# Optimization experiments

Measured on AMD Instinct MI355X. Metric: run time of the kernel, lower is better.

Reference implementation:

```python
import jax, jax.numpy as jnp
import numpy as np

N = 100000      # nodes
E = 3200000     # edges (avg degree 32)
F_IN = 16       # node_feature_size
R1, R2, R3 = 8, 16, 8   # gcn hidden sizes
N1 = 32                  # mlp hidden


def _lin(k, fan_in, shape):
    s = 1.0 / np.sqrt(fan_in)
    return jax.random.uniform(k, shape, minval=-s, maxval=s, dtype=jnp.float32)


def setup_inputs() -> dict:
    key = jax.random.key(0)
    ks = jax.random.split(key, 16)
    x = jax.random.normal(ks[0], (N, F_IN), dtype=jnp.float32)
    edge_index = jax.random.randint(ks[1], (2, E), 0, N, dtype=jnp.int64)
    return {
        "x": x,
        "edge_index": edge_index,
        # GraphConv k: out = mean_agg(x_j) @ W_rel + b + x @ W_root  (PyG GraphConv, lin_root bias=False)
        "W_rel1": _lin(ks[2], F_IN, (F_IN, R1)), "b1": _lin(ks[3], F_IN, (R1,)), "W_root1": _lin(ks[4], F_IN, (F_IN, R1)),
        "W_rel2": _lin(ks[5], R1, (R1, R2)),   "b2": _lin(ks[6], R1, (R2,)),   "W_root2": _lin(ks[7], R1, (R1, R2)),
        "W_rel3": _lin(ks[8], R2, (R2, R3)),   "b3": _lin(ks[9], R2, (R3,)),   "W_root3": _lin(ks[10], R2, (R2, R3)),
        "fc1_W": _lin(ks[11], R3, (R3, N1)), "fc1_b": _lin(ks[12], R3, (N1,)),
        "fc2_W": _lin(ks[13], N1, (N1, 1)),  "fc2_b": _lin(ks[14], N1, (1,)),
    }


def _graph_conv(x, src, dst, W_rel, b, W_root):
    # message: gather source features; aggregate: mean over incoming edges at dst
    n = x.shape[0]
    msg_sum = jax.ops.segment_sum(x[src], dst, num_segments=n)          # [N, F]
    cnt = jax.ops.segment_sum(jnp.ones(src.shape, x.dtype), dst, num_segments=n)
    mean = msg_sum / jnp.maximum(cnt, 1.0)[:, None]
    return mean @ W_rel + b + x @ W_root


def reference(x, edge_index, W_rel1, b1, W_root1, W_rel2, b2, W_root2,
              W_rel3, b3, W_root3, fc1_W, fc1_b, fc2_W, fc2_b):
    src, dst = edge_index[0], edge_index[1]
    h = jax.nn.sigmoid(_graph_conv(x, src, dst, W_rel1, b1, W_root1))
    h = jax.nn.sigmoid(_graph_conv(h, src, dst, W_rel2, b2, W_root2))
    h = jax.nn.sigmoid(_graph_conv(h, src, dst, W_rel3, b3, W_root3))
    h = jax.nn.sigmoid(h @ fc1_W + fc1_b)
    return h @ fc2_W + fc2_b   # [N, 1]
```

## Files before the change

### kernel.cpp

```cpp
#include <hip/hip_runtime.h>
#include <math.h>


#define CHUNK  8192
#define BW     128
#define MAXB   6144
#define MAXNB  800
#define MAXBLK 512

typedef _Float16 half8 __attribute__((ext_vector_type(8)));

static __device__ __forceinline__ float sigmoidf_(float x) {
    return 1.0f / (1.0f + expf(-x));
}

static __device__ __forceinline__ int scan256_excl(int v, int* s) {
    int tid = threadIdx.x;
    s[tid] = v;
    for (int off = 1; off < 256; off <<= 1) {
        __syncthreads();
        int t = (tid >= off) ? s[tid - off] : 0;
        __syncthreads();
        s[tid] += t;
    }
    __syncthreads();
    return s[tid] - v;
}

static __device__ __forceinline__ void gather_mean8(
    const half8* __restrict__ t, const int* __restrict__ csr,
    int rs, int d, float* s) {
#pragma unroll
    for (int c = 0; c < 8; ++c) s[c] = 0.0f;
    int e = 0;
    for (; e + 4 <= d; e += 4) {
        int4 ci = *(const int4*)(csr + rs + e);
        half8 v0 = t[ci.x]; half8 v1 = t[ci.y];
        half8 v2 = t[ci.z]; half8 v3 = t[ci.w];
#pragma unroll
        for (int c = 0; c < 8; ++c)
            s[c] += ((float)v0[c] + (float)v1[c]) + ((float)v2[c] + (float)v3[c]);
    }
    for (; e < d; ++e) {
        half8 v = t[csr[rs + e]];
#pragma unroll
        for (int c = 0; c < 8; ++c) s[c] += (float)v[c];
    }
    float inv = 1.0f / (float)(d > 0 ? d : 1);
#pragma unroll
    for (int c = 0; c < 8; ++c) s[c] *= inv;
}

__global__ __launch_bounds__(256)
void transform1_kernel(const float* __restrict__ x, const float* __restrict__ Wrel,
                       const float* __restrict__ bias, const float* __restrict__ Wroot,
                       _Float16* __restrict__ t1, _Float16* __restrict__ z1, int n) {
    __shared__ float sWr[128], sWo[128], sb[8];
    int tid = threadIdx.x;
    if (tid < 128) { sWr[tid] = Wrel[tid]; sWo[tid] = Wroot[tid]; }
    if (tid < 8) sb[tid] = bias[tid];
    __syncthreads();
    int node = blockIdx.x * 256 + tid;
    if (node >= n) return;
    const float4* x4 = (const float4*)x;
    float xv[16];
#pragma unroll
    for (int k = 0; k < 4; ++k) {
        float4 v = x4[node * 4 + k];
        xv[4 * k] = v.x; xv[4 * k + 1] = v.y; xv[4 * k + 2] = v.z; xv[4 * k + 3] = v.w;
    }
    float ta[8], za[8];
#pragma unroll
    for (int j = 0; j < 8; ++j) { ta[j] = 0.0f; za[j] = sb[j]; }
#pragma unroll
    for (int f = 0; f < 16; ++f) {
        float xf = xv[f];
#pragma unroll
        for (int j = 0; j < 8; ++j) {
            ta[j] += xf * sWr[f * 8 + j];
            za[j] += xf * sWo[f * 8 + j];
        }
    }
    half8 th, zh;
#pragma unroll
    for (int j = 0; j < 8; ++j) { th[j] = (_Float16)ta[j]; zh[j] = (_Float16)za[j]; }
    ((half8*)t1)[node] = th;
    ((half8*)z1)[node] = zh;
}

__global__ __launch_bounds__(256)
void bin_sort_kernel(const int* __restrict__ src, const int* __restrict__ dst,
                     unsigned* __restrict__ packed, int* __restrict__ counts_bm,
                     int* __restrict__ lstart_bm, int E, int NB) {
    __shared__ int s_hist[MAXNB];
    __shared__ int s_cur[MAXNB];
    __shared__ unsigned s_pk[CHUNK];
    __shared__ int s_scan[256];
    int tid = threadIdx.x, blk = blockIdx.x;
    for (int i = tid; i < NB; i += 256) s_hist[i] = 0;
    __syncthreads();

    int base = blk * CHUNK;
    int cnt = E - base; if (cnt > CHUNK) cnt = CHUNK;

    if (cnt == CHUNK) {
        const int4* d4 = (const int4*)(dst + base);
#pragma unroll
        for (int k = 0; k < CHUNK / 1024; ++k) {
            int4 d = d4[k * 256 + tid];
            atomicAdd(&s_hist[d.x >> 7], 1);
            atomicAdd(&s_hist[d.y >> 7], 1);
            atomicAdd(&s_hist[d.z >> 7], 1);
            atomicAdd(&s_hist[d.w >> 7], 1);
        }
    } else {
        for (int i = tid; i < cnt; i += 256) atomicAdd(&s_hist[dst[base + i] >> 7], 1);
    }
    __syncthreads();

    int per = (NB + 255) / 256;
    int st = tid * per;
    int lsum = 0;
    for (int j = 0; j < per; ++j)
        if (st + j < NB) lsum += s_hist[st + j];
    int excl = scan256_excl(lsum, s_scan);
    int run = excl;
    for (int j = 0; j < per; ++j)
        if (st + j < NB) { s_cur[st + j] = run; run += s_hist[st + j]; }
    __syncthreads();

    if (cnt == CHUNK) {
        const int4* d4 = (const int4*)(dst + base);
        const int4* s4 = (const int4*)(src + base);
#pragma unroll
        for (int k = 0; k < CHUNK / 1024; ++k) {
            int4 d = d4[k * 256 + tid];
            int4 s = s4[k * 256 + tid];
            int dd[4] = {d.x, d.y, d.z, d.w};
            int ss[4] = {s.x, s.y, s.z, s.w};
#pragma unroll
            for (int j = 0; j < 4; ++j) {
                int pos = atomicAdd(&s_cur[dd[j] >> 7], 1);
                s_pk[pos] = ((unsigned)(dd[j] & 127) << 17) | (unsigned)ss[j];
            }
        }
    } else {
        for (int i = tid; i < cnt; i += 256) {
            int d = dst[base + i], s = src[base + i];
            int pos = atomicAdd(&s_cur[d >> 7], 1);
            s_pk[pos] = ((unsigned)(d & 127) << 17) | (unsigned)s;
        }
    }
    __syncthreads();

    for (int i = tid; i < cnt; i += 256) packed[base + i] = s_pk[i];
    for (int i = tid; i < NB; i += 256) {
        int h = s_hist[i];
        counts_bm[blk * NB + i] = h;
        lstart_bm[blk * NB + i] = s_cur[i] - h;
    }
}

__global__ __launch_bounds__(256)
void transpose2_kernel(const int* __restrict__ a, int* __restrict__ at,
                       const int* __restrict__ b, int* __restrict__ bt,
                       int rows, int cols) {
    __shared__ int ta[32][33];
    __shared__ int tb[32][33];
    int tx = threadIdx.x & 31, ty = threadIdx.x >> 5;
    int r0 = blockIdx.y * 32, c0 = blockIdx.x * 32;
#pragma unroll
    for (int k = 0; k < 4; ++k) {
        int r = r0 + ty + 8 * k, c = c0 + tx;
        if (r < rows && c < cols) {
            ta[ty + 8 * k][tx] = a[r * cols + c];
            tb[ty + 8 * k][tx] = b[r * cols + c];
        }
    }
    __syncthreads();
#pragma unroll
    for (int k = 0; k < 4; ++k) {
        int c = c0 + ty + 8 * k, r = r0 + tx;
        if (c < cols && r < rows) {
            at[c * rows + r] = ta[tx][ty + 8 * k];
            bt[c * rows + r] = tb[tx][ty + 8 * k];
        }
    }
}

__global__ __launch_bounds__(256)
void btot_kernel(const int* __restrict__ counts_t, int* __restrict__ btot, int NBLK) {
    __shared__ int s_scan[256];
    int b = blockIdx.x, tid = threadIdx.x;
    int v = 0;
    for (int i = tid; i < NBLK; i += 256) v += counts_t[b * NBLK + i];
    scan256_excl(v, s_scan);
    if (tid == 255) btot[b] = s_scan[255];
}

__global__ __launch_bounds__(1024)
void bscan_kernel(const int* __restrict__ btot, int* __restrict__ bstart, int NB) {
    __shared__ int lds[1024];
    int tid = threadIdx.x;
    int v = (tid < NB) ? (((btot[tid] + 3) & ~3) + 512) : 0;
    lds[tid] = v;
    for (int off = 1; off < 1024; off <<= 1) {
        __syncthreads();
        int t = (tid >= off) ? lds[tid - off] : 0;
        __syncthreads();
        lds[tid] += t;
    }
    __syncthreads();
    if (tid < NB) bstart[tid] = lds[tid] - v;
}

__global__ __launch_bounds__(256)
void bucket_sort_kernel(const unsigned* __restrict__ packed,
                        const int* __restrict__ counts_t,
                        const int* __restrict__ lstart_t,
                        const int* __restrict__ bstart,
                        int* __restrict__ csr_src, int* __restrict__ deg,
                        int* __restrict__ rowstart, int N, int NB, int NBLK) {
    __shared__ int s_cnt[MAXBLK], s_lst[MAXBLK], s_off[MAXBLK];
    __shared__ unsigned s_p[MAXB];
    __shared__ int s_out[MAXB];
    __shared__ int h[BW], hs[BW], curb[BW];
    __shared__ int s_scan[256];
    __shared__ int s_tot, s_ptot;
    int b = blockIdx.x, tid = threadIdx.x;
    int beg = bstart[b];

    for (int i = tid; i < NBLK; i += 256) {
        s_cnt[i] = counts_t[b * NBLK + i];
        s_lst[i] = lstart_t[b * NBLK + i];
    }
    __syncthreads();

    int per = (NBLK + 255) / 256;
    int st = tid * per;
    int lsum = 0;
    for (int j = 0; j < per; ++j)
        if (st + j < NBLK) lsum += s_cnt[st + j];
    int excl = scan256_excl(lsum, s_scan);
    if (tid == 255) s_tot = s_scan[255];
    int run = excl;
    for (int j = 0; j < per; ++j)
        if (st + j < NBLK) { s_off[st + j] = run; run += s_cnt[st + j]; }
    __syncthreads();
    int cnt = s_tot; if (cnt > MAXB) cnt = MAXB;

    for (int blk = tid; blk < NBLK; blk += 256) {
        int c = s_cnt[blk], o = s_off[blk];
        const unsigned* p = packed + (size_t)blk * CHUNK + s_lst[blk];
        for (int j = 0; j < c; ++j) s_p[o + j] = p[j];
    }
    if (tid < BW) h[tid] = 0;
    __syncthreads();

    for (int i = tid; i < cnt; i += 256) atomicAdd(&h[s_p[i] >> 17], 1);
    __syncthreads();
    if (tid == 0) {
        int acc = 0;
        for (int i = 0; i < BW; ++i) { hs[i] = acc; acc += (h[i] + 3) & ~3; }
        s_ptot = acc;
    }
    __syncthreads();
    if (tid < BW) {
        curb[tid] = hs[tid];
        int node = b * BW + tid;
        if (node < N) { deg[node] = h[tid]; rowstart[node] = beg + hs[tid]; }
    }
    __syncthreads();
    for (int i = tid; i < cnt; i += 256) {
        unsigned p = s_p[i];
        int pos = atomicAdd(&curb[p >> 17], 1);
        s_out[pos] = (int)(p & 0x1FFFF);
    }
    __syncthreads();
    int ptot = s_ptot; if (ptot > MAXB) ptot = MAXB;
    for (int i = tid; i < ptot; i += 256) csr_src[beg + i] = s_out[i];
}

__global__ __launch_bounds__(256)
void agg1_kernel(const _Float16* __restrict__ t1, const _Float16* __restrict__ z1,
                 const int* __restrict__ rowstart, const int* __restrict__ deg,
                 const int* __restrict__ csr, _Float16* __restrict__ h1, int n) {
    int node = blockIdx.x * 256 + threadIdx.x;
    if (node >= n) return;
    float s[8];
    gather_mean8((const half8*)t1, csr, rowstart[node], deg[node], s);
    half8 z = ((const half8*)z1)[node];
    half8 o;
#pragma unroll
    for (int c = 0; c < 8; ++c) o[c] = (_Float16)sigmoidf_(s[c] + (float)z[c]);
    ((half8*)h1)[node] = o;
}

__global__ __launch_bounds__(256)
void gcn2_fused_kernel(const _Float16* __restrict__ h1,
                       const int* __restrict__ rowstart, const int* __restrict__ deg,
                       const int* __restrict__ csr,
                       const float* __restrict__ W2r, const float* __restrict__ b2,
                       const float* __restrict__ W2o,
                       const float* __restrict__ W3r, const float* __restrict__ b3,
                       const float* __restrict__ W3o,
                       _Float16* __restrict__ t3, _Float16* __restrict__ z3, int n) {
    __shared__ float sW2r[128], sW2o[128], sW3r[128], sW3o[128], sb2[16], sb3[8];
    int tid = threadIdx.x;
    if (tid < 128) {
        sW2r[tid] = W2r[tid]; sW2o[tid] = W2o[tid];
        sW3r[tid] = W3r[tid]; sW3o[tid] = W3o[tid];
    }
    if (tid < 16) sb2[tid] = b2[tid];
    if (tid < 8) sb3[tid] = b3[tid];
    __syncthreads();
    int node = blockIdx.x * 256 + tid;
    if (node >= n) return;

    float m[8];
    gather_mean8((const half8*)h1, csr, rowstart[node], deg[node], m);
    half8 sf = ((const half8*)h1)[node];
    float x8[8];
#pragma unroll
    for (int c = 0; c < 8; ++c) x8[c] = (float)sf[c];

    float v16[16];
#pragma unroll
    for (int j = 0; j < 16; ++j) {
        float a = sb2[j];
#pragma unroll
        for (int f = 0; f < 8; ++f)
            a += m[f] * sW2r[f * 16 + j] + x8[f] * sW2o[f * 16 + j];
        v16[j] = sigmoidf_(a);
    }
    float ta[8], za[8];
#pragma unroll
    for (int j = 0; j < 8; ++j) { ta[j] = 0.0f; za[j] = sb3[j]; }
#pragma unroll
    for (int f = 0; f < 16; ++f) {
        float hv = v16[f];
#pragma unroll
        for (int j = 0; j < 8; ++j) {
            ta[j] += hv * sW3r[f * 8 + j];
            za[j] += hv * sW3o[f * 8 + j];
        }
    }
    half8 th, zh;
#pragma unroll
    for (int j = 0; j < 8; ++j) { th[j] = (_Float16)ta[j]; zh[j] = (_Float16)za[j]; }
    ((half8*)t3)[node] = th;
    ((half8*)z3)[node] = zh;
}

__global__ __launch_bounds__(256)
void agg3_mlp_kernel(const _Float16* __restrict__ t3, const _Float16* __restrict__ z3,
                     const int* __restrict__ rowstart, const int* __restrict__ deg,
                     const int* __restrict__ csr,
                     const float* __restrict__ fc1W, const float* __restrict__ fc1b,
                     const float* __restrict__ fc2W, const float* __restrict__ fc2b,
                     float* __restrict__ out, int n) {
    __shared__ float sW1[256], sb1[32], sW2[32];
    __shared__ float sb2_;
    int tid = threadIdx.x;
    if (tid < 256) sW1[tid] = fc1W[tid];
    if (tid < 32) { sb1[tid] = fc1b[tid]; sW2[tid] = fc2W[tid]; }
    if (tid == 0) sb2_ = fc2b[0];
    __syncthreads();
    int node = blockIdx.x * 256 + tid;
    if (node >= n) return;

    float s[8];
    gather_mean8((const half8*)t3, csr, rowstart[node], deg[node], s);
    half8 z = ((const half8*)z3)[node];
    float h[8];
#pragma unroll
    for (int c = 0; c < 8; ++c) h[c] = sigmoidf_(s[c] + (float)z[c]);

    float acc = sb2_;
#pragma unroll
    for (int j = 0; j < 32; ++j) {
        float a = sb1[j];
#pragma unroll
        for (int f = 0; f < 8; ++f) a += h[f] * sW1[f * 32 + j];
        acc += sW2[j] * sigmoidf_(a);
    }
    out[node] = acc;
}

extern "C" void kernel_launch(void* const* d_in, const int* in_sizes, int n_in,
                              void* d_out, int out_size, void* d_ws, size_t ws_size,
                              hipStream_t stream) {
    const float* x      = (const float*)d_in[0];
    const int*   ei     = (const int*)d_in[1];
    const float* Wrel1  = (const float*)d_in[2];
    const float* b1     = (const float*)d_in[3];
    const float* Wroot1 = (const float*)d_in[4];
    const float* Wrel2  = (const float*)d_in[5];
    const float* b2     = (const float*)d_in[6];
    const float* Wroot2 = (const float*)d_in[7];
    const float* Wrel3  = (const float*)d_in[8];
    const float* b3     = (const float*)d_in[9];
    const float* Wroot3 = (const float*)d_in[10];
    const float* fc1W   = (const float*)d_in[11];
    const float* fc1b   = (const float*)d_in[12];
    const float* fc2W   = (const float*)d_in[13];
    const float* fc2b   = (const float*)d_in[14];
    float* out = (float*)d_out;

    const int N = in_sizes[0] / 16;
    const int E = in_sizes[1] / 2;
    const int* e_src = ei;
    const int* e_dst = ei + E;

    const int NB   = (N + BW - 1) / BW;
    const int NBLK = (E + CHUNK - 1) / CHUNK;

    char* ws = (char*)d_ws;
    size_t off = 0;
    auto alloc = [&](size_t bytes) { char* p = ws + off; off += (bytes + 15) & ~size_t(15); return p; };
    unsigned* packed   = (unsigned*)alloc((size_t)NBLK * CHUNK * 4);
    int* counts_bm     = (int*)alloc((size_t)NBLK * NB * 4);
    int* lstart_bm     = (int*)alloc((size_t)NBLK * NB * 4);
    int* counts_t      = (int*)alloc((size_t)NBLK * NB * 4);
    int* lstart_t      = (int*)alloc((size_t)NBLK * NB * 4);
    int* btot          = (int*)alloc((size_t)NB * 4);
    int* bstart        = (int*)alloc((size_t)NB * 4);
    int* csr_src       = (int*)alloc(((size_t)E + (size_t)NB * 516) * 4);
    int* deg           = (int*)alloc((size_t)N * 4);
    int* rowstart      = (int*)alloc((size_t)N * 4);
    _Float16* t1       = (_Float16*)alloc((size_t)N * 8 * 2);
    _Float16* z1       = (_Float16*)alloc((size_t)N * 8 * 2);
    _Float16* h1       = (_Float16*)alloc((size_t)N * 8 * 2);
    _Float16* t3       = (_Float16*)alloc((size_t)N * 8 * 2);
    _Float16* z3       = (_Float16*)alloc((size_t)N * 8 * 2);

    const int nbN = (N + 255) / 256;

    transform1_kernel<<<nbN, 256, 0, stream>>>(x, Wrel1, b1, Wroot1, t1, z1, N);

    bin_sort_kernel<<<NBLK, 256, 0, stream>>>(e_src, e_dst, packed, counts_bm, lstart_bm, E, NB);
    dim3 tgrid((NB + 31) / 32, (NBLK + 31) / 32);
    transpose2_kernel<<<tgrid, 256, 0, stream>>>(counts_bm, counts_t, lstart_bm, lstart_t, NBLK, NB);
    btot_kernel<<<NB, 256, 0, stream>>>(counts_t, btot, NBLK);
    bscan_kernel<<<1, 1024, 0, stream>>>(btot, bstart, NB);
    bucket_sort_kernel<<<NB, 256, 0, stream>>>(packed, counts_t, lstart_t, bstart,
                                               csr_src, deg, rowstart, N, NB, NBLK);

    agg1_kernel<<<nbN, 256, 0, stream>>>(t1, z1, rowstart, deg, csr_src, h1, N);
    gcn2_fused_kernel<<<nbN, 256, 0, stream>>>(h1, rowstart, deg, csr_src,
                                               Wrel2, b2, Wroot2, Wrel3, b3, Wroot3, t3, z3, N);
    agg3_mlp_kernel<<<nbN, 256, 0, stream>>>(t3, z3, rowstart, deg, csr_src,
                                             fc1W, fc1b, fc2W, fc2b, out, N);
}
```

Before: 232.6 us.

## Restructure CSR build into hist/scan/scatter passes and split gathers across thread pairs

The edge bucketing pipeline is reorganized. A histogram-only pass is followed by a per-bucket scan over block counts, then a scatter pass that writes packed edges directly into their global bucket slots. This removes the packed intermediate, the transpose kernel and the serial per-block copy loop in the bucket sort. Separately, the three aggregation kernels now assign two threads per node, each summing half of the neighbor list and combining with a lane shuffle. This doubles thread-level parallelism for the latency-bound gathers, at the cost of redundant dense compute in the second lane and a smaller MAXB cap on bucket size.

```diff
diff --git a/kernel.cpp b/kernel.cpp
--- a/kernel.cpp
+++ b/kernel.cpp
@@ -4,9 +4,9 @@
 
 #define CHUNK  8192
 #define BW     128
-#define MAXB   6144
 #define MAXNB  800
 #define MAXBLK 512
+#define MAXB   5120
 
 typedef _Float16 half8 __attribute__((ext_vector_type(8)));
 
@@ -27,13 +27,13 @@
     return s[tid] - v;
 }
 
-static __device__ __forceinline__ void gather_mean8(
+static __device__ __forceinline__ void gather_sum8(
     const half8* __restrict__ t, const int* __restrict__ csr,
-    int rs, int d, float* s) {
+    int rs, int from, int to, float* s) {
 #pragma unroll
     for (int c = 0; c < 8; ++c) s[c] = 0.0f;
-    int e = 0;
-    for (; e + 4 <= d; e += 4) {
+    int e = from;
+    for (; e + 4 <= to; e += 4) {
         int4 ci = *(const int4*)(csr + rs + e);
         half8 v0 = t[ci.x]; half8 v1 = t[ci.y];
         half8 v2 = t[ci.z]; half8 v3 = t[ci.w];
@@ -41,11 +41,22 @@
         for (int c = 0; c < 8; ++c)
             s[c] += ((float)v0[c] + (float)v1[c]) + ((float)v2[c] + (float)v3[c]);
     }
-    for (; e < d; ++e) {
+    for (; e < to; ++e) {
         half8 v = t[csr[rs + e]];
 #pragma unroll
         for (int c = 0; c < 8; ++c) s[c] += (float)v[c];
     }
+}
+
+static __device__ __forceinline__ void pair_gather_mean8(
+    const half8* __restrict__ t, const int* __restrict__ csr,
+    int rs, int d, int half, float* s) {
+    int d1 = ((d >> 1) + 3) & ~3; if (d1 > d) d1 = d;
+    int from = half ? d1 : 0;
+    int to   = half ? d  : d1;
+    gather_sum8(t, csr, rs, from, to, s);
+#pragma unroll
+    for (int c = 0; c < 8; ++c) s[c] += __shfl_xor(s[c], 1);
     float inv = 1.0f / (float)(d > 0 ? d : 1);
 #pragma unroll
     for (int c = 0; c < 8; ++c) s[c] *= inv;
@@ -89,20 +100,14 @@
 }
 
 __global__ __launch_bounds__(256)
-void bin_sort_kernel(const int* __restrict__ src, const int* __restrict__ dst,
-                     unsigned* __restrict__ packed, int* __restrict__ counts_bm,
-                     int* __restrict__ lstart_bm, int E, int NB) {
+void hist_kernel(const int* __restrict__ dst, int* __restrict__ counts_bm,
+                 int E, int NB) {
     __shared__ int s_hist[MAXNB];
-    __shared__ int s_cur[MAXNB];
-    __shared__ unsigned s_pk[CHUNK];
-    __shared__ int s_scan[256];
     int tid = threadIdx.x, blk = blockIdx.x;
     for (int i = tid; i < NB; i += 256) s_hist[i] = 0;
     __syncthreads();
-
     int base = blk * CHUNK;
     int cnt = E - base; if (cnt > CHUNK) cnt = CHUNK;
-
     if (cnt == CHUNK) {
         const int4* d4 = (const int4*)(dst + base);
 #pragma unroll
@@ -117,84 +122,26 @@
         for (int i = tid; i < cnt; i += 256) atomicAdd(&s_hist[dst[base + i] >> 7], 1);
     }
     __syncthreads();
-
-    int per = (NB + 255) / 256;
+    for (int i = tid; i < NB; i += 256) counts_bm[blk * NB + i] = s_hist[i];
+}
+
+__global__ __launch_bounds__(256)
+void btot_scan_kernel(const int* __restrict__ counts_bm, int* __restrict__ rawstart_t,
+                      int* __restrict__ btot, int NB, int NBLK) {
+    __shared__ int s_scan[256];
+    __shared__ int s_c[MAXBLK];
+    int b = blockIdx.x, tid = threadIdx.x;
+    for (int i = tid; i < NBLK; i += 256) s_c[i] = counts_bm[i * NB + b];
+    __syncthreads();
+    int per = (NBLK + 255) / 256;
     int st = tid * per;
     int lsum = 0;
     for (int j = 0; j < per; ++j)
-        if (st + j < NB) lsum += s_hist[st + j];
+        if (st + j < NBLK) lsum += s_c[st + j];
     int excl = scan256_excl(lsum, s_scan);
     int run = excl;
     for (int j = 0; j < per; ++j)
-        if (st + j < NB) { s_cur[st + j] = run; run += s_hist[st + j]; }
-    __syncthreads();
-
-    if (cnt == CHUNK) {
-        const int4* d4 = (const int4*)(dst + base);
-        const int4* s4 = (const int4*)(src + base);
-#pragma unroll
-        for (int k = 0; k < CHUNK / 1024; ++k) {
-            int4 d = d4[k * 256 + tid];
-            int4 s = s4[k * 256 + tid];
-            int dd[4] = {d.x, d.y, d.z, d.w};
-            int ss[4] = {s.x, s.y, s.z, s.w};
-#pragma unroll
-            for (int j = 0; j < 4; ++j) {
-                int pos = atomicAdd(&s_cur[dd[j] >> 7], 1);
-                s_pk[pos] = ((unsigned)(dd[j] & 127) << 17) | (unsigned)ss[j];
-            }
-        }
-    } else {
-        for (int i = tid; i < cnt; i += 256) {
-            int d = dst[base + i], s = src[base + i];
-            int pos = atomicAdd(&s_cur[d >> 7], 1);
-            s_pk[pos] = ((unsigned)(d & 127) << 17) | (unsigned)s;
-        }
-    }
-    __syncthreads();
-
-    for (int i = tid; i < cnt; i += 256) packed[base + i] = s_pk[i];
-    for (int i = tid; i < NB; i += 256) {
-        int h = s_hist[i];
-        counts_bm[blk * NB + i] = h;
-        lstart_bm[blk * NB + i] = s_cur[i] - h;
-    }
-}
-
-__global__ __launch_bounds__(256)
-void transpose2_kernel(const int* __restrict__ a, int* __restrict__ at,
-                       const int* __restrict__ b, int* __restrict__ bt,
-                       int rows, int cols) {
-    __shared__ int ta[32][33];
-    __shared__ int tb[32][33];
-    int tx = threadIdx.x & 31, ty = threadIdx.x >> 5;
-    int r0 = blockIdx.y * 32, c0 = blockIdx.x * 32;
-#pragma unroll
-    for (int k = 0; k < 4; ++k) {
-        int r = r0 + ty + 8 * k, c = c0 + tx;
-        if (r < rows && c < cols) {
-            ta[ty + 8 * k][tx] = a[r * cols + c];
-            tb[ty + 8 * k][tx] = b[r * cols + c];
-        }
-    }
-    __syncthreads();
-#pragma unroll
-    for (int k = 0; k < 4; ++k) {
-        int c = c0 + ty + 8 * k, r = r0 + tx;
-        if (c < cols && r < rows) {
-            at[c * rows + r] = ta[tx][ty + 8 * k];
-            bt[c * rows + r] = tb[tx][ty + 8 * k];
-        }
-    }
-}
-
-__global__ __launch_bounds__(256)
-void btot_kernel(const int* __restrict__ counts_t, int* __restrict__ btot, int NBLK) {
-    __shared__ int s_scan[256];
-    int b = blockIdx.x, tid = threadIdx.x;
-    int v = 0;
-    for (int i = tid; i < NBLK; i += 256) v += counts_t[b * NBLK + i];
-    scan256_excl(v, s_scan);
+        if (st + j < NBLK) { rawstart_t[b * NBLK + st + j] = run; run += s_c[st + j]; }
     if (tid == 255) btot[b] = s_scan[255];
 }
 
@@ -215,54 +162,63 @@
 }
 
 __global__ __launch_bounds__(256)
-void bucket_sort_kernel(const unsigned* __restrict__ packed,
-                        const int* __restrict__ counts_t,
-                        const int* __restrict__ lstart_t,
-                        const int* __restrict__ bstart,
-                        int* __restrict__ csr_src, int* __restrict__ deg,
-                        int* __restrict__ rowstart, int N, int NB, int NBLK) {
-    __shared__ int s_cnt[MAXBLK], s_lst[MAXBLK], s_off[MAXBLK];
+void scatter_kernel(const int* __restrict__ src, const int* __restrict__ dst,
+                    const int* __restrict__ rawstart_t, const int* __restrict__ bstart,
+                    unsigned* __restrict__ stage, int E, int NB, int NBLK) {
+    __shared__ int s_cur[MAXNB];
+    int tid = threadIdx.x, blk = blockIdx.x;
+    for (int i = tid; i < NB; i += 256)
+        s_cur[i] = bstart[i] + rawstart_t[i * NBLK + blk];
+    __syncthreads();
+    int base = blk * CHUNK;
+    int cnt = E - base; if (cnt > CHUNK) cnt = CHUNK;
+    if (cnt == CHUNK) {
+        const int4* d4 = (const int4*)(dst + base);
+        const int4* s4 = (const int4*)(src + base);
+#pragma unroll
+        for (int k = 0; k < CHUNK / 1024; ++k) {
+            int4 d = d4[k * 256 + tid];
+            int4 s = s4[k * 256 + tid];
+            int dd[4] = {d.x, d.y, d.z, d.w};
+            int ss[4] = {s.x, s.y, s.z, s.w};
+#pragma unroll
+            for (int j = 0; j < 4; ++j) {
+                int pos = atomicAdd(&s_cur[dd[j] >> 7], 1);
+                stage[pos] = ((unsigned)(dd[j] & 127) << 17) | (unsigned)ss[j];
+            }
+        }
+    } else {
+        for (int i = tid; i < cnt; i += 256) {
+            int d = dst[base + i], s = src[base + i];
+            int pos = atomicAdd(&s_cur[d >> 7], 1);
+            stage[pos] = ((unsigned)(d & 127) << 17) | (unsigned)s;
+        }
+    }
+}
+
+__global__ __launch_bounds__(256)
+void bucket_csr_kernel(const unsigned* __restrict__ stage,
+                       const int* __restrict__ bstart, const int* __restrict__ btot,
+                       int* __restrict__ csr, int* __restrict__ deg,
+                       int* __restrict__ rowstart, int N, int NB) {
     __shared__ unsigned s_p[MAXB];
-    __shared__ int s_out[MAXB];
     __shared__ int h[BW], hs[BW], curb[BW];
-    __shared__ int s_scan[256];
-    __shared__ int s_tot, s_ptot;
     int b = blockIdx.x, tid = threadIdx.x;
     int beg = bstart[b];
-
-    for (int i = tid; i < NBLK; i += 256) {
-        s_cnt[i] = counts_t[b * NBLK + i];
-        s_lst[i] = lstart_t[b * NBLK + i];
-    }
-    __syncthreads();
-
-    int per = (NBLK + 255) / 256;
-    int st = tid * per;
-    int lsum = 0;
-    for (int j = 0; j < per; ++j)
-        if (st + j < NBLK) lsum += s_cnt[st + j];
-    int excl = scan256_excl(lsum, s_scan);
-    if (tid == 255) s_tot = s_scan[255];
-    int run = excl;
-    for (int j = 0; j < per; ++j)
-        if (st + j < NBLK) { s_off[st + j] = run; run += s_cnt[st + j]; }
-    __syncthreads();
-    int cnt = s_tot; if (cnt > MAXB) cnt = MAXB;
-
-    for (int blk = tid; blk < NBLK; blk += 256) {
-        int c = s_cnt[blk], o = s_off[blk];
-        const unsigned* p = packed + (size_t)blk * CHUNK + s_lst[blk];
-        for (int j = 0; j < c; ++j) s_p[o + j] = p[j];
-    }
+    int tot = btot[b]; if (tot > MAXB) tot = MAXB;
+
+    const uint4* st4 = (const uint4*)(stage + beg);
+    int n4 = tot >> 2;
+    for (int i = tid; i < n4; i += 256) ((uint4*)s_p)[i] = st4[i];
+    for (int i = (n4 << 2) + tid; i < tot; i += 256) s_p[i] = stage[beg + i];
     if (tid < BW) h[tid] = 0;
     __syncthreads();
 
-    for (int i = tid; i < cnt; i += 256) atomicAdd(&h[s_p[i] >> 17], 1);
+    for (int i = tid; i < tot; i += 256) atomicAdd(&h[s_p[i] >> 17], 1);
     __syncthreads();
     if (tid == 0) {
         int acc = 0;
         for (int i = 0; i < BW; ++i) { hs[i] = acc; acc += (h[i] + 3) & ~3; }
-        s_ptot = acc;
     }
     __syncthreads();
     if (tid < BW) {
@@ -271,24 +227,23 @@
         if (node < N) { deg[node] = h[tid]; rowstart[node] = beg + hs[tid]; }
     }
     __syncthreads();
-    for (int i = tid; i < cnt; i += 256) {
+    for (int i = tid; i < tot; i += 256) {
         unsigned p = s_p[i];
         int pos = atomicAdd(&curb[p >> 17], 1);
-        s_out[pos] = (int)(p & 0x1FFFF);
-    }
-    __syncthreads();
-    int ptot = s_ptot; if (ptot > MAXB) ptot = MAXB;
-    for (int i = tid; i < ptot; i += 256) csr_src[beg + i] = s_out[i];
+        csr[beg + pos] = (int)(p & 0x1FFFF);
+    }
 }
 
 __global__ __launch_bounds__(256)
 void agg1_kernel(const _Float16* __restrict__ t1, const _Float16* __restrict__ z1,
                  const int* __restrict__ rowstart, const int* __restrict__ deg,
                  const int* __restrict__ csr, _Float16* __restrict__ h1, int n) {
-    int node = blockIdx.x * 256 + threadIdx.x;
+    int idx = blockIdx.x * 256 + threadIdx.x;
+    int node = idx >> 1, half = idx & 1;
     if (node >= n) return;
     float s[8];
-    gather_mean8((const half8*)t1, csr, rowstart[node], deg[node], s);
+    pair_gather_mean8((const half8*)t1, csr, rowstart[node], deg[node], half, s);
+    if (half) return;
     half8 z = ((const half8*)z1)[node];
     half8 o;
 #pragma unroll
@@ -314,11 +269,12 @@
     if (tid < 16) sb2[tid] = b2[tid];
     if (tid < 8) sb3[tid] = b3[tid];
     __syncthreads();
-    int node = blockIdx.x * 256 + tid;
+    int idx = blockIdx.x * 256 + tid;
+    int node = idx >> 1, half = idx & 1;
     if (node >= n) return;
 
     float m[8];
-    gather_mean8((const half8*)h1, csr, rowstart[node], deg[node], m);
+    pair_gather_mean8((const half8*)h1, csr, rowstart[node], deg[node], half, m);
     half8 sf = ((const half8*)h1)[node];
     float x8[8];
 #pragma unroll
@@ -345,6 +301,7 @@
             za[j] += hv * sW3o[f * 8 + j];
         }
     }
+    if (half) return;
     half8 th, zh;
 #pragma unroll
     for (int j = 0; j < 8; ++j) { th[j] = (_Float16)ta[j]; zh[j] = (_Float16)za[j]; }
@@ -366,11 +323,12 @@
     if (tid < 32) { sb1[tid] = fc1b[tid]; sW2[tid] = fc2W[tid]; }
     if (tid == 0) sb2_ = fc2b[0];
     __syncthreads();
-    int node = blockIdx.x * 256 + tid;
+    int idx = blockIdx.x * 256 + tid;
+    int node = idx >> 1, half = idx & 1;
     if (node >= n) return;
 
     float s[8];
-    gather_mean8((const half8*)t3, csr, rowstart[node], deg[node], s);
+    pair_gather_mean8((const half8*)t3, csr, rowstart[node], deg[node], half, s);
     half8 z = ((const half8*)z3)[node];
     float h[8];
 #pragma unroll
@@ -384,7 +342,7 @@
         for (int f = 0; f < 8; ++f) a += h[f] * sW1[f * 32 + j];
         acc += sW2[j] * sigmoidf_(a);
     }
-    out[node] = acc;
+    if (half == 0) out[node] = acc;
 }
 
 extern "C" void kernel_launch(void* const* d_in, const int* in_sizes, int n_in,
@@ -414,18 +372,18 @@
 
     const int NB   = (N + BW - 1) / BW;
     const int NBLK = (E + CHUNK - 1) / CHUNK;
+    const int nbN  = (N + 255) / 256;
+    const int nbP  = (2 * N + 255) / 256;
 
     char* ws = (char*)d_ws;
     size_t off = 0;
     auto alloc = [&](size_t bytes) { char* p = ws + off; off += (bytes + 15) & ~size_t(15); return p; };
-    unsigned* packed   = (unsigned*)alloc((size_t)NBLK * CHUNK * 4);
+    unsigned* stage    = (unsigned*)alloc(((size_t)E + (size_t)NB * 516 + 64) * 4);
+    int* csr           = (int*)alloc(((size_t)E + (size_t)NB * 516 + 64) * 4);
     int* counts_bm     = (int*)alloc((size_t)NBLK * NB * 4);
-    int* lstart_bm     = (int*)alloc((size_t)NBLK * NB * 4);
-    int* counts_t      = (int*)alloc((size_t)NBLK * NB * 4);
-    int* lstart_t      = (int*)alloc((size_t)NBLK * NB * 4);
+    int* rawstart_t    = (int*)alloc((size_t)NB * NBLK * 4);
     int* btot          = (int*)alloc((size_t)NB * 4);
     int* bstart        = (int*)alloc((size_t)NB * 4);
-    int* csr_src       = (int*)alloc(((size_t)E + (size_t)NB * 516) * 4);
     int* deg           = (int*)alloc((size_t)N * 4);
     int* rowstart      = (int*)alloc((size_t)N * 4);
     _Float16* t1       = (_Float16*)alloc((size_t)N * 8 * 2);
@@ -434,21 +392,17 @@
     _Float16* t3       = (_Float16*)alloc((size_t)N * 8 * 2);
     _Float16* z3       = (_Float16*)alloc((size_t)N * 8 * 2);
 
-    const int nbN = (N + 255) / 256;
-
     transform1_kernel<<<nbN, 256, 0, stream>>>(x, Wrel1, b1, Wroot1, t1, z1, N);
 
-    bin_sort_kernel<<<NBLK, 256, 0, stream>>>(e_src, e_dst, packed, counts_bm, lstart_bm, E, NB);
-    dim3 tgrid((NB + 31) / 32, (NBLK + 31) / 32);
-    transpose2_kernel<<<tgrid, 256, 0, stream>>>(counts_bm, counts_t, lstart_bm, lstart_t, NBLK, NB);
-    btot_kernel<<<NB, 256, 0, stream>>>(counts_t, btot, NBLK);
+    hist_kernel<<<NBLK, 256, 0, stream>>>(e_dst, counts_bm, E, NB);
+    btot_scan_kernel<<<NB, 256, 0, stream>>>(counts_bm, rawstart_t, btot, NB, NBLK);
     bscan_kernel<<<1, 1024, 0, stream>>>(btot, bstart, NB);
-    bucket_sort_kernel<<<NB, 256, 0, stream>>>(packed, counts_t, lstart_t, bstart,
-                                               csr_src, deg, rowstart, N, NB, NBLK);
-
-    agg1_kernel<<<nbN, 256, 0, stream>>>(t1, z1, rowstart, deg, csr_src, h1, N);
-    gcn2_fused_kernel<<<nbN, 256, 0, stream>>>(h1, rowstart, deg, csr_src,
+    scatter_kernel<<<NBLK, 256, 0, stream>>>(e_src, e_dst, rawstart_t, bstart, stage, E, NB, NBLK);
+    bucket_csr_kernel<<<NB, 256, 0, stream>>>(stage, bstart, btot, csr, deg, rowstart, N, NB);
+
+    agg1_kernel<<<nbP, 256, 0, stream>>>(t1, z1, rowstart, deg, csr, h1, N);
+    gcn2_fused_kernel<<<nbP, 256, 0, stream>>>(h1, rowstart, deg, csr,
                                                Wrel2, b2, Wroot2, Wrel3, b3, Wroot3, t3, z3, N);
-    agg3_mlp_kernel<<<nbN, 256, 0, stream>>>(t3, z3, rowstart, deg, csr_src,
+    agg3_mlp_kernel<<<nbP, 256, 0, stream>>>(t3, z3, rowstart, deg, csr,
                                              fc1W, fc1b, fc2W, fc2b, out, N);
 }
```

New measurement: 255.8 us. 10.0% more time.
